# Performance work log

Measured on AMD Instinct MI355X. Metric: run time of the kernel, lower is better.

## Reference

```python
import jax, jax.numpy as jnp
import numpy as np
from jax import lax

B, C, H, W = 2048, 3, 64, 64
NUM_NODES = 20
N = B * NUM_NODES


def _edges():
    # fully-connected (no self loop) 20-node graph, replicated per batch element
    i, j = np.meshgrid(np.arange(NUM_NODES), np.arange(NUM_NODES), indexing='ij')
    m = i != j
    src, dst = i[m], j[m]  # 380 edges per graph
    off = (np.arange(B) * NUM_NODES)[:, None]
    rows = (src[None] + off).reshape(-1)
    cols = (dst[None] + off).reshape(-1)
    return jnp.asarray(np.stack([rows, cols]), dtype=jnp.int32)  # [2, B*380]


def setup_inputs() -> dict:
    key = jax.random.key(0)
    ks = jax.random.split(key, 8)
    return dict(
        im=jax.random.uniform(ks[0], (B, C, H, W), jnp.float32),
        x=jax.random.normal(ks[1], (N, 2), jnp.float32),
        edge_index=_edges(),
        conv1_w=jax.random.normal(ks[2], (10, 3, 11, 11), jnp.float32) * 0.05,
        conv2_w=jax.random.normal(ks[3], (16, 10, 5, 5), jnp.float32) * 0.05,
        conv2_b=jnp.zeros((16,), jnp.float32),
        lin_w=jax.random.normal(ks[4], (2, 64), jnp.float32) * 0.1,
        lin_b=jnp.zeros((2,), jnp.float32),
        g1_w=jax.random.normal(ks[5], (8, 4), jnp.float32) * 0.3,
        g1_b=jnp.zeros((8,), jnp.float32),
        g2_w=jax.random.normal(ks[6], (1, 8), jnp.float32) * 0.3,
        g2_b=jnp.zeros((1,), jnp.float32),
    )


def _maxpool(h, k, s):
    return lax.reduce_window(h, -jnp.inf, lax.max, (1, 1, k, k), (1, 1, s, s), 'VALID')


def _gcn(x, edge_index, Wt, b, improved, aggr):
    # PyG GCNConv: linear (no bias) -> gcn_norm with self-loops -> scatter aggr -> +bias
    x = x @ Wt.T
    n = x.shape[0]
    fill = 2.0 if improved else 1.0  # improved adds self-loop weight 2
    loop = jnp.arange(n, dtype=edge_index.dtype)
    row = jnp.concatenate([edge_index[0], loop])  # source (flow=source_to_target)
    col = jnp.concatenate([edge_index[1], loop])  # target
    ew = jnp.concatenate([jnp.ones(edge_index.shape[1], x.dtype), jnp.full((n,), fill, x.dtype)])
    deg = jax.ops.segment_sum(ew, col, num_segments=n)
    dis = jnp.where(deg > 0, lax.rsqrt(jnp.maximum(deg, 1e-12)), 0.0)
    norm = dis[row] * ew * dis[col]
    msg = norm[:, None] * x[row]  # gather + weight
    if aggr == 'mean':
        s = jax.ops.segment_sum(msg, col, num_segments=n)
        cnt = jax.ops.segment_sum(jnp.ones_like(norm), col, num_segments=n)
        out = s / jnp.maximum(cnt, 1.0)[:, None]
    else:  # max
        out = jax.ops.segment_max(msg, col, num_segments=n)
        out = jnp.where(jnp.isfinite(out), out, 0.0)
    return out + b


def reference(im, x, edge_index, conv1_w, conv2_w, conv2_b, lin_w, lin_b, g1_w, g1_b, g2_w, g2_b):
    dn = ('NCHW', 'OIHW', 'NCHW')
    h = lax.conv_general_dilated(im, conv1_w, (4, 4), [(2, 2), (2, 2)], dimension_numbers=dn)
    h = jax.nn.leaky_relu(h)          # slope 0.01, matches nn.LeakyReLU default
    h = _maxpool(h, 3, 2)             # [B,10,7,7]
    h = lax.conv_general_dilated(h, conv2_w, (2, 2), [(2, 2), (2, 2)], dimension_numbers=dn)
    h = h + conv2_b[None, :, None, None]
    h = jax.nn.leaky_relu(h)
    h = _maxpool(h, 2, 2)             # [B,16,2,2]
    h = h.reshape(-1, 64)
    img_feat = jax.nn.sigmoid(h @ lin_w.T + lin_b)  # [B,2]
    xin = jnp.concatenate([x, jnp.repeat(img_feat, NUM_NODES, axis=0)], axis=1)  # [N,4]
    h1 = jax.nn.leaky_relu(_gcn(xin, edge_index, g1_w, g1_b, False, 'mean'))
    h2 = _gcn(h1, edge_index, g2_w, g2_b, True, 'max')  # [N,1]
    out = jax.nn.softmax(h2.reshape(B, NUM_NODES), axis=1)
    return out, img_feat
```

## Files before the change

### kernel.cpp

```cpp
#include <hip/hip_runtime.h>
#include <hip/hip_bf16.h>
#include <math.h>


#define PLW 72
#define PLANE_SH (PLW * 68)
#define OUT1_OFF 9792
#define SMEM_BYTES (OUT1_OFF + 2250 * 4)

typedef __attribute__((ext_vector_type(8))) short bf16x8;
typedef __attribute__((ext_vector_type(4))) float f32x4;

__device__ inline unsigned short f2bf(float f) {
    unsigned u = __float_as_uint(f);
    u += 0x7fff + ((u >> 16) & 1);
    return (unsigned short)(u >> 16);
}

__global__ void reorder_weights(const float* __restrict__ w1,
                                const float* __restrict__ w2,
                                unsigned char* __restrict__ ws) {
    unsigned short* bN = (unsigned short*)ws;
    unsigned short* bS = (unsigned short*)(ws + 18432);
    float* w2t = (float*)(ws + 36864);
    const int id = blockIdx.x * 256 + threadIdx.x;
    for (int e = id; e < 9216; e += 4096) {
        int j = e & 7, lane = (e >> 3) & 63, s = e >> 9;
        int n = lane & 15, q = lane >> 4;
        int c = s / 6, kyp = s - c * 6;
        int k = q * 8 + j;
        int ky = 2 * kyp + (k >> 4);
        int kxN = k & 15, kxS = (k & 15) - 4;
        unsigned short vN = 0, vS = 0;
        if (n < 10 && ky < 11) {
            const float* wr = w1 + n * 363 + c * 121 + ky * 11;
            if (kxN < 11) vN = f2bf(wr[kxN]);
            if (kxS >= 0 && kxS < 11) vS = f2bf(wr[kxS]);
        }
        bN[e] = vN;
        bS[e] = vS;
    }
    for (int i = id; i < 4000; i += 4096) {
        int k = i & 15, tap = i >> 4;
        w2t[i] = w2[k * 250 + tap];
    }
}

__global__ __launch_bounds__(256) void cnn_mfma(
        const float* __restrict__ im,
        const unsigned char* __restrict__ wsb,
        const float* __restrict__ conv2_b,
        const float* __restrict__ lin_w,
        const float* __restrict__ lin_b,
        float* __restrict__ out) {
    __shared__ __align__(16) unsigned char smem[SMEM_BYTES];
    unsigned short* plane = (unsigned short*)smem;
    float* smemf = (float*)smem;
    float* out1 = (float*)(smem + OUT1_OFF);
    const int b = blockIdx.x, t = threadIdx.x;
    const int lane = t & 63, wid = t >> 6;
    const int n = lane & 15, q = lane >> 4;

    if (t < 20) out[b * 20 + t] = 0.05f;

    for (int i = t; i < PLANE_SH / 4; i += 256)
        ((unsigned long long*)plane)[i] = 0ull;

    const bool even_cls = (wid < 2);
    const int nt = (wid == 3) ? 3 : 4;
    const int t0 = (wid & 1) * 4;
    const unsigned short* bfr =
        (const unsigned short*)(wsb + (even_cls ? 0 : 18432));

    const int lofs = (q >> 1) * 72 + (q & 1) * 8;
    int ebase[4];
#pragma unroll
    for (int tl = 0; tl < 4; ++tl) {
        int Tl = t0 + ((tl < nt) ? tl : 0);
        int i = Tl * 16 + n;
        int oy, cb;
        if (even_cls) {
            oy = min(i >> 3, 14);
            cb = (i & 7) << 3;
        } else {
            int oyu = i / 7, rem = i - oyu * 7;
            oy = min(oyu, 14);
            cb = rem << 3;
        }
        ebase[tl] = 288 * oy + cb + lofs;
    }

    f32x4 acc[4];
#pragma unroll
    for (int i = 0; i < 4; ++i) acc[i] = (f32x4)(0.0f);

    for (int c = 0; c < 3; ++c) {
        __syncthreads();
        const float4* imc = (const float4*)(im + ((size_t)(b * 3 + c)) * 4096);
#pragma unroll
        for (int jj = 0; jj < 4; ++jj) {
            int ii = t + jj * 256;
            float4 v = imc[ii];
            int y = ii >> 4, x4 = (ii & 15) << 2;
            int e = (y + 2) * PLW + x4 + 2;
            *(__hip_bfloat162*)(&plane[e]) =
                __float22bfloat162_rn(make_float2(v.x, v.y));
            *(__hip_bfloat162*)(&plane[e + 2]) =
                __float22bfloat162_rn(make_float2(v.z, v.w));
        }
        __syncthreads();
        const unsigned short* bsl = bfr + c * 3072 + lane * 8;
#pragma unroll 1
        for (int kyp = 0; kyp < 6; ++kyp) {
            bf16x8 bf = *(const bf16x8*)(bsl + kyp * 512);
            const int ro = kyp * 144;
#pragma unroll
            for (int tl = 0; tl < 4; ++tl) {
                if (tl < nt) {
                    bf16x8 a = *(const bf16x8*)(&plane[ebase[tl] + ro]);
                    acc[tl] = __builtin_amdgcn_mfma_f32_16x16x32_bf16(
                        a, bf, acc[tl], 0, 0, 0);
                }
            }
        }
    }

    __syncthreads();
#pragma unroll
    for (int tl = 0; tl < 4; ++tl) {
        if (tl < nt) {
            int Tl = t0 + tl;
#pragma unroll
            for (int r = 0; r < 4; ++r) {
                int i = Tl * 16 + (q << 2) + r;
                float v = acc[tl][r];
                v = v > 0.0f ? v : 0.01f * v;
                if (n < 10) {
                    if (even_cls) {
                        if (i < 120) out1[n * 225 + (i >> 3) * 15 + ((i & 7) << 1)] = v;
                    } else {
                        if (i < 105) {
                            int oyu = i / 7;
                            out1[n * 225 + oyu * 15 + (i - oyu * 7) * 2 + 1] = v;
                        }
                    }
                }
            }
        }
    }
    float* p1p = smemf;
    for (int i = t; i < 1210; i += 256) p1p[i] = 0.0f;
    __syncthreads();
    for (int i = t; i < 490; i += 256) {
        int c2 = i / 49, r = (i % 49) / 7, col = i % 7;
        const float* o1 = &out1[c2 * 225 + (2 * r) * 15 + 2 * col];
        float m = o1[0];
        m = fmaxf(m, o1[1]);  m = fmaxf(m, o1[2]);
        m = fmaxf(m, o1[15]); m = fmaxf(m, o1[16]); m = fmaxf(m, o1[17]);
        m = fmaxf(m, o1[30]); m = fmaxf(m, o1[31]); m = fmaxf(m, o1[32]);
        p1p[c2 * 121 + (r + 2) * 11 + (col + 2)] = m;
    }
    __syncthreads();
    {
        const float* w2t = (const float*)(wsb + 36864);
        const int pix2 = lane >> 2, kg = lane & 3;
        const int o2y = pix2 >> 2, o2x = pix2 & 3;
        const int c2s = (wid * 10) >> 2, c2e = ((wid + 1) * 10) >> 2;
        float ax = 0.f, ay = 0.f, az = 0.f, aw = 0.f;
#pragma unroll 1
        for (int c2 = c2s; c2 < c2e; ++c2) {
#pragma unroll
            for (int ky = 0; ky < 5; ++ky) {
#pragma unroll
                for (int kx = 0; kx < 5; ++kx) {
                    float v = p1p[c2 * 121 + (o2y * 2 + ky) * 11 + o2x * 2 + kx];
                    float4 w = *(const float4*)(w2t + (c2 * 25 + ky * 5 + kx) * 16 + kg * 4);
                    ax = fmaf(v, w.x, ax); ay = fmaf(v, w.y, ay);
                    az = fmaf(v, w.z, az); aw = fmaf(v, w.w, aw);
                }
            }
        }
        *(float4*)(&smemf[1216 + wid * 256 + pix2 * 16 + kg * 4]) =
            make_float4(ax, ay, az, aw);
    }
    __syncthreads();
    float* out2 = smemf + 2240;
    float* hbuf = smemf + 2496;
    {
        const int k = t & 15, pix = t >> 4;
        float s = smemf[1216 + pix * 16 + k] + smemf[1472 + pix * 16 + k] +
                  smemf[1728 + pix * 16 + k] + smemf[1984 + pix * 16 + k];
        s += conv2_b[k];
        s = s > 0.0f ? s : 0.01f * s;
        out2[k * 16 + pix] = s;
    }
    __syncthreads();
    if (t < 64) {
        int k = t >> 2, qy = (t >> 1) & 1, qx = t & 1;
        const float* o2 = &out2[k * 16 + (2 * qy) * 4 + 2 * qx];
        hbuf[t] = fmaxf(fmaxf(o2[0], o2[1]), fmaxf(o2[4], o2[5]));
    }
    __syncthreads();
    if (t < 128) {
        int o = t >> 6, l = t & 63;
        float p = hbuf[l] * lin_w[o * 64 + l];
#pragma unroll
        for (int m = 32; m >= 1; m >>= 1) p += __shfl_xor(p, m);
        if (l == 0)
            out[40960 + b * 2 + o] = 1.0f / (1.0f + expf(-(p + lin_b[o])));
    }
}

__global__ __launch_bounds__(256) void cnn_fallback(
        const float* __restrict__ im, const float* __restrict__ w1,
        const float* __restrict__ w2, const float* __restrict__ conv2_b,
        const float* __restrict__ lin_w, const float* __restrict__ lin_b,
        float* __restrict__ out) {
    __shared__ __align__(16) float bufA[68 * 68];
    const int b = blockIdx.x, t = threadIdx.x;
    if (t < 20) out[b * 20 + t] = 0.05f;
    for (int i = t; i < 68 * 68; i += 256) bufA[i] = 0.0f;
    float acc[10];
#pragma unroll
    for (int i = 0; i < 10; ++i) acc[i] = 0.0f;
    const int oy = min(t / 15, 14), ox = t % 15;
    for (int c = 0; c < 3; ++c) {
        __syncthreads();
        const float4* imc = (const float4*)(im + ((size_t)(b * 3 + c)) * 4096);
        for (int i = t; i < 1024; i += 256) {
            float4 v = imc[i];
            int y = i >> 4, x4 = (i & 15) << 2;
            float* dst = &bufA[(y + 2) * 68 + x4 + 2];
            dst[0] = v.x; dst[1] = v.y; dst[2] = v.z; dst[3] = v.w;
        }
        __syncthreads();
#pragma unroll 1
        for (int ky = 0; ky < 11; ++ky) {
            const float* row = &bufA[(oy * 4 + ky) * 68 + ox * 4];
            float4 r0 = *(const float4*)(row);
            float4 r1 = *(const float4*)(row + 4);
            float4 r2 = *(const float4*)(row + 8);
            float in[12] = {r0.x, r0.y, r0.z, r0.w, r1.x, r1.y, r1.z, r1.w,
                            r2.x, r2.y, r2.z, r2.w};
#pragma unroll
            for (int kx = 0; kx < 11; ++kx) {
                float v = in[kx];
#pragma unroll
                for (int oc = 0; oc < 10; ++oc)
                    acc[oc] = fmaf(v, w1[oc * 363 + c * 121 + ky * 11 + kx], acc[oc]);
            }
        }
    }
    __syncthreads();
    if (t < 225) {
#pragma unroll
        for (int oc = 0; oc < 10; ++oc) {
            float v = acc[oc];
            bufA[oc * 225 + t] = v > 0.0f ? v : 0.01f * v;
        }
    }
    float* p1p = bufA + 3100;
    for (int i = t; i < 1210; i += 256) p1p[i] = 0.0f;
    __syncthreads();
    for (int i = t; i < 490; i += 256) {
        int c2 = i / 49, r = (i % 49) / 7, col = i % 7;
        const float* o1 = &bufA[c2 * 225 + (2 * r) * 15 + 2 * col];
        float m = o1[0];
        m = fmaxf(m, o1[1]);  m = fmaxf(m, o1[2]);
        m = fmaxf(m, o1[15]); m = fmaxf(m, o1[16]); m = fmaxf(m, o1[17]);
        m = fmaxf(m, o1[30]); m = fmaxf(m, o1[31]); m = fmaxf(m, o1[32]);
        p1p[c2 * 121 + (r + 2) * 11 + (col + 2)] = m;
    }
    __syncthreads();
    float* out2 = bufA;
    float* hbuf = bufA + 256;
    {
        const int k = t & 15, pix = t >> 4;
        const int o2y = pix >> 2, o2x = pix & 3;
        float a2 = 0.0f;
#pragma unroll 1
        for (int c2 = 0; c2 < 10; ++c2)
#pragma unroll
            for (int ky = 0; ky < 5; ++ky)
#pragma unroll
                for (int kx = 0; kx < 5; ++kx) {
                    float v = p1p[c2 * 121 + (o2y * 2 + ky) * 11 + o2x * 2 + kx];
                    a2 = fmaf(v, w2[k * 250 + c2 * 25 + ky * 5 + kx], a2);
                }
        a2 += conv2_b[k];
        a2 = a2 > 0.0f ? a2 : 0.01f * a2;
        __syncthreads();
        out2[k * 16 + pix] = a2;
    }
    __syncthreads();
    if (t < 64) {
        int k = t >> 2, qy = (t >> 1) & 1, qx = t & 1;
        const float* o2 = &out2[k * 16 + (2 * qy) * 4 + 2 * qx];
        hbuf[t] = fmaxf(fmaxf(o2[0], o2[1]), fmaxf(o2[4], o2[5]));
    }
    __syncthreads();
    if (t < 128) {
        int o = t >> 6, l = t & 63;
        float p = hbuf[l] * lin_w[o * 64 + l];
#pragma unroll
        for (int m = 32; m >= 1; m >>= 1) p += __shfl_xor(p, m);
        if (l == 0)
            out[40960 + b * 2 + o] = 1.0f / (1.0f + expf(-(p + lin_b[o])));
    }
}

extern "C" void kernel_launch(void* const* d_in, const int* in_sizes, int n_in,
                              void* d_out, int out_size, void* d_ws, size_t ws_size,
                              hipStream_t stream) {
    const float* im = (const float*)d_in[0];
    const float* w1 = (const float*)d_in[3];
    const float* w2 = (const float*)d_in[4];
    const float* b2 = (const float*)d_in[5];
    const float* lw = (const float*)d_in[6];
    const float* lb = (const float*)d_in[7];
    float* out = (float*)d_out;

    if (ws_size >= 52864) {
        reorder_weights<<<16, 256, 0, stream>>>(w1, w2, (unsigned char*)d_ws);
        cnn_mfma<<<2048, 256, 0, stream>>>(im, (const unsigned char*)d_ws,
                                           b2, lw, lb, out);
    } else {
        cnn_fallback<<<2048, 256, 0, stream>>>(im, w1, w2, b2, lw, lb, out);
    }
}
```

Baseline: 191.8 us.

## Double-buffer input channel planes and prefetch weights in conv1 MFMA loop

Conv1 now uses two bf16 input planes. The next channel is staged while MFMAs run on the current one, which cuts one barrier per channel. B-fragment weights are prefetched one iteration ahead, and only the padding borders of the planes and the pooled buffer are zeroed instead of the whole buffers. The maxpool-to-linear step is folded into the dot-product threads to drop a barrier, and launch bounds request 8 blocks per CU. LDS use grows to two planes (about 19.6KB), which may limit occupancy, and the border-only zeroing must cover every cell the MFMA reads.

```diff
diff --git a/kernel.cpp b/kernel.cpp
--- a/kernel.cpp
+++ b/kernel.cpp
@@ -5,8 +5,8 @@
 
 #define PLW 72
 #define PLANE_SH (PLW * 68)
-#define OUT1_OFF 9792
-#define SMEM_BYTES (OUT1_OFF + 2250 * 4)
+#define PLANE_B (PLANE_SH * 2)
+#define SMEM_BYTES (2 * PLANE_B)
 
 typedef __attribute__((ext_vector_type(8))) short bf16x8;
 typedef __attribute__((ext_vector_type(4))) float f32x4;
@@ -46,7 +46,22 @@
     }
 }
 
-__global__ __launch_bounds__(256) void cnn_mfma(
+__device__ inline void stage_channel(const float4* __restrict__ imc,
+                                     unsigned short* __restrict__ dst, int t) {
+#pragma unroll
+    for (int jj = 0; jj < 4; ++jj) {
+        int ii = t + jj * 256;
+        float4 v = imc[ii];
+        int y = ii >> 4, x4 = (ii & 15) << 2;
+        int e = (y + 2) * PLW + x4 + 2;
+        *(__hip_bfloat162*)(&dst[e]) =
+            __float22bfloat162_rn(make_float2(v.x, v.y));
+        *(__hip_bfloat162*)(&dst[e + 2]) =
+            __float22bfloat162_rn(make_float2(v.z, v.w));
+    }
+}
+
+__global__ __launch_bounds__(256, 8) void cnn_mfma(
         const float* __restrict__ im,
         const unsigned char* __restrict__ wsb,
         const float* __restrict__ conv2_b,
@@ -56,21 +71,19 @@
     __shared__ __align__(16) unsigned char smem[SMEM_BYTES];
     unsigned short* plane = (unsigned short*)smem;
     float* smemf = (float*)smem;
-    float* out1 = (float*)(smem + OUT1_OFF);
     const int b = blockIdx.x, t = threadIdx.x;
     const int lane = t & 63, wid = t >> 6;
     const int n = lane & 15, q = lane >> 4;
 
     if (t < 20) out[b * 20 + t] = 0.05f;
-
-    for (int i = t; i < PLANE_SH / 4; i += 256)
-        ((unsigned long long*)plane)[i] = 0ull;
 
     const bool even_cls = (wid < 2);
     const int nt = (wid == 3) ? 3 : 4;
     const int t0 = (wid & 1) * 4;
     const unsigned short* bfr =
         (const unsigned short*)(wsb + (even_cls ? 0 : 18432));
+    const unsigned short* bsl = bfr + lane * 8;
+    bf16x8 bf = *(const bf16x8*)(bsl);
 
     const int lofs = (q >> 1) * 72 + (q & 1) * 8;
     int ebase[4];
@@ -94,26 +107,36 @@
 #pragma unroll
     for (int i = 0; i < 4; ++i) acc[i] = (f32x4)(0.0f);
 
+    stage_channel((const float4*)(im + ((size_t)(b * 3)) * 4096), plane, t);
+
+    for (int i = t; i < 528; i += 256) {
+        int p = (i >= 264) ? 1 : 0;
+        int s = i - p * 264;
+        unsigned short* pl = plane + p * PLANE_SH;
+        if (s < 72) {
+            int rr = s / 18, cu = s - rr * 18;
+            int r = (rr < 2) ? rr : (64 + rr);
+            *((unsigned long long*)(pl + r * PLW) + cu) = 0ull;
+        } else {
+            int s2 = s - 72;
+            int r = 2 + s2 / 3, j = s2 - (s2 / 3) * 3;
+            unsigned short* row = pl + r * PLW;
+            if (j == 0)      *(unsigned int*)(row) = 0u;
+            else if (j == 1) *(unsigned int*)(row + 66) = 0u;
+            else             *(unsigned long long*)(row + 68) = 0ull;
+        }
+    }
+    __syncthreads();
+
     for (int c = 0; c < 3; ++c) {
-        __syncthreads();
-        const float4* imc = (const float4*)(im + ((size_t)(b * 3 + c)) * 4096);
-#pragma unroll
-        for (int jj = 0; jj < 4; ++jj) {
-            int ii = t + jj * 256;
-            float4 v = imc[ii];
-            int y = ii >> 4, x4 = (ii & 15) << 2;
-            int e = (y + 2) * PLW + x4 + 2;
-            *(__hip_bfloat162*)(&plane[e]) =
-                __float22bfloat162_rn(make_float2(v.x, v.y));
-            *(__hip_bfloat162*)(&plane[e + 2]) =
-                __float22bfloat162_rn(make_float2(v.z, v.w));
-        }
-        __syncthreads();
-        const unsigned short* bsl = bfr + c * 3072 + lane * 8;
+        if (c < 2)
+            stage_channel((const float4*)(im + ((size_t)(b * 3 + c + 1)) * 4096),
+                          plane + (((c & 1) ^ 1) ? PLANE_SH : 0), t);
+        const int pbase = (c & 1) * PLANE_SH;
 #pragma unroll 1
         for (int kyp = 0; kyp < 6; ++kyp) {
-            bf16x8 bf = *(const bf16x8*)(bsl + kyp * 512);
-            const int ro = kyp * 144;
+            bf16x8 bfn = *(const bf16x8*)(bsl + (c * 6 + kyp + 1) * 512);
+            const int ro = pbase + kyp * 144;
 #pragma unroll
             for (int tl = 0; tl < 4; ++tl) {
                 if (tl < nt) {
@@ -122,10 +145,12 @@
                         a, bf, acc[tl], 0, 0, 0);
                 }
             }
-        }
-    }
-
-    __syncthreads();
+            bf = bfn;
+        }
+        if (c < 2) __syncthreads();
+    }
+
+    float* out1 = (float*)(smem + PLANE_B);
 #pragma unroll
     for (int tl = 0; tl < 4; ++tl) {
         if (tl < nt) {
@@ -148,19 +173,35 @@
             }
         }
     }
+    __syncthreads();
+
     float* p1p = smemf;
-    for (int i = t; i < 1210; i += 256) p1p[i] = 0.0f;
-    __syncthreads();
     for (int i = t; i < 490; i += 256) {
-        int c2 = i / 49, r = (i % 49) / 7, col = i % 7;
-        const float* o1 = &out1[c2 * 225 + (2 * r) * 15 + 2 * col];
+        int c2 = i / 49, rr = (i % 49) / 7, col = i % 7;
+        const float* o1 = &out1[c2 * 225 + (2 * rr) * 15 + 2 * col];
         float m = o1[0];
         m = fmaxf(m, o1[1]);  m = fmaxf(m, o1[2]);
         m = fmaxf(m, o1[15]); m = fmaxf(m, o1[16]); m = fmaxf(m, o1[17]);
         m = fmaxf(m, o1[30]); m = fmaxf(m, o1[31]); m = fmaxf(m, o1[32]);
-        p1p[c2 * 121 + (r + 2) * 11 + (col + 2)] = m;
-    }
-    __syncthreads();
+        p1p[c2 * 121 + (rr + 2) * 11 + (col + 2)] = m;
+    }
+    for (int i = t; i < 720; i += 256) {
+        int c2 = i / 72, r = i - c2 * 72;
+        int row, col;
+        if (r < 44) {
+            int rr = r / 11;
+            row = (rr < 2) ? rr : 7 + rr;
+            col = r - rr * 11;
+        } else {
+            int r2 = r - 44;
+            row = 2 + (r2 >> 2);
+            int cc = r2 & 3;
+            col = (cc < 2) ? cc : 7 + cc;
+        }
+        p1p[c2 * 121 + row * 11 + col] = 0.0f;
+    }
+    __syncthreads();
+
     {
         const float* w2t = (const float*)(wsb + 36864);
         const int pix2 = lane >> 2, kg = lane & 3;
@@ -185,7 +226,6 @@
     }
     __syncthreads();
     float* out2 = smemf + 2240;
-    float* hbuf = smemf + 2496;
     {
         const int k = t & 15, pix = t >> 4;
         float s = smemf[1216 + pix * 16 + k] + smemf[1472 + pix * 16 + k] +
@@ -195,15 +235,12 @@
         out2[k * 16 + pix] = s;
     }
     __syncthreads();
-    if (t < 64) {
-        int k = t >> 2, qy = (t >> 1) & 1, qx = t & 1;
-        const float* o2 = &out2[k * 16 + (2 * qy) * 4 + 2 * qx];
-        hbuf[t] = fmaxf(fmaxf(o2[0], o2[1]), fmaxf(o2[4], o2[5]));
-    }
-    __syncthreads();
     if (t < 128) {
         int o = t >> 6, l = t & 63;
-        float p = hbuf[l] * lin_w[o * 64 + l];
+        int k = l >> 2, qy = (l >> 1) & 1, qx = l & 1;
+        const float* o2 = &out2[k * 16 + (2 * qy) * 4 + 2 * qx];
+        float hb = fmaxf(fmaxf(o2[0], o2[1]), fmaxf(o2[4], o2[5]));
+        float p = hb * lin_w[o * 64 + l];
 #pragma unroll
         for (int m = 32; m >= 1; m >>= 1) p += __shfl_xor(p, m);
         if (l == 0)
```

Result: slower. 207.9 us (+8.4%).
